# Kernel tuning notes

Hardware: AMD Instinct MI355X
Metric: run time of the kernel (lower is better)

The kernel has to match this reference:

```python
import jax, jax.numpy as jnp
import numpy as np

B, N, D, H, R, K = 64, 197, 768, 3072, 16, 1


def setup_inputs() -> dict:
    key = jax.random.key(0)
    ks = jax.random.split(key, 9)
    s1 = 1.0 / np.sqrt(D)
    s2 = 1.0 / np.sqrt(H)
    return {
        "x": jax.random.normal(ks[0], (B, N, D), dtype=jnp.float32),
        "W1": jax.random.normal(ks[1], (H, D), dtype=jnp.float32) * s1,
        "b1": jax.random.normal(ks[2], (H,), dtype=jnp.float32) * s1,
        "A1": jax.random.normal(ks[3], (K, R, D), dtype=jnp.float32) * s1,
        "B1": jax.random.normal(ks[4], (K, H, R), dtype=jnp.float32) * 0.01,
        "W2": jax.random.normal(ks[5], (D, H), dtype=jnp.float32) * s2,
        "b2": jax.random.normal(ks[6], (D,), dtype=jnp.float32) * s2,
        "A2": jax.random.normal(ks[7], (K, R, H), dtype=jnp.float32) * s2,
        "B2": jax.random.normal(ks[8], (K, D, R), dtype=jnp.float32) * 0.01,
    }


def _lora(x, A, Bm):
    # result of torch: (B @ (A @ x^T.unsqueeze(1))).sum(1).transpose(1,2)
    # A: [K, r, d_in], Bm: [K, d_out, r], x: [b, n, d_in] -> [b, n, d_out]
    t = jnp.einsum('krd,bnd->bknr', A, x)          # low-rank projection
    return jnp.einsum('kor,bknr->bno', Bm, t)      # expand + sum over K


def reference(x, W1, b1, A1, B1, W2, b2, A2, B2):
    # fc1 (Linear + LoRA correction)
    h = jnp.einsum('bnd,hd->bnh', x, W1) + b1 + _lora(x, A1, B1)
    # exact (erf-based) GELU, matching torch nn.GELU default
    h = jax.nn.gelu(h, approximate=False)
    # dropout p=0 and norm=Identity by default -> no-ops
    out = jnp.einsum('bnh,dh->bnd', h, W2) + b2 + _lora(h, A2, B2)
    return out
```

## Files before the change

kernel.cpp:

```cpp
#include <hip/hip_runtime.h>
#include <math.h>

#define M_ROWS 12608
#define D_DIM  768
#define H_DIM  3072

typedef __bf16 bf16_t;
typedef __bf16 bf16x8 __attribute__((ext_vector_type(8)));
typedef float  f32x4  __attribute__((ext_vector_type(4)));

__device__ __forceinline__ float gelu_fast(float v) {
  float v2 = v * v;
  float z = v * fmaf(0.044715f, v2, 1.0f);
  float e = __expf(-1.5957691216057308f * z);
  return v * __builtin_amdgcn_rcpf(1.0f + e);
}

__device__ __forceinline__ void gld16(const bf16_t* g, char* l) {
  __builtin_amdgcn_global_load_lds(
      (const __attribute__((address_space(1))) void*)g,
      (__attribute__((address_space(3))) void*)l, 16, 0, 0);
}

__global__ void cast_f32_bf16_kernel(const float* __restrict__ in,
                                     bf16_t* __restrict__ out, long n) {
  long i = ((long)blockIdx.x * 256 + threadIdx.x) * 4;
  if (i + 3 < n) {
    float4 v = *(const float4*)(in + i);
    out[i + 0] = (bf16_t)v.x; out[i + 1] = (bf16_t)v.y;
    out[i + 2] = (bf16_t)v.z; out[i + 3] = (bf16_t)v.w;
  } else {
    for (; i < n; ++i) out[i] = (bf16_t)in[i];
  }
}

__global__ void fold_lora_kernel(const float* __restrict__ W,
                                 const float* __restrict__ A,
                                 const float* __restrict__ Bm,
                                 bf16_t* __restrict__ Weff,
                                 int OUT, int IN) {
  long idx = (long)blockIdx.x * 256 + threadIdx.x;
  if (idx >= (long)OUT * IN) return;
  int o = (int)(idx / IN);
  int i = (int)(idx - (long)o * IN);
  float s = W[idx];
#pragma unroll
  for (int r = 0; r < 16; ++r)
    s += Bm[o * 16 + r] * A[r * IN + i];
  Weff[idx] = (bf16_t)s;
}

template <bool GELU, typename OutT, int SCHED, int SMEM_BYTES>
__global__ __launch_bounds__(256, 3) void gemm_kernel(
    const bf16_t* __restrict__ Amat, const bf16_t* __restrict__ Bmat,
    const float* __restrict__ bias, OutT* __restrict__ Cmat,
    int Mrows, int Ncols, int Kd) {
  __shared__ char smem[SMEM_BYTES];
  bf16_t* lds = (bf16_t*)smem;
  float* sT = (float*)smem;

  int rowb, colb;
  const int xcd = blockIdx.x & 7, t = blockIdx.x >> 3;
  if (SCHED == 1) {
    colb = t / 13;
    rowb = (t % 13) * 8 + xcd;
    if (rowb >= 99) return;
  } else {
    rowb = (t / 3) * 4 + (xcd & 3);
    if (rowb >= 99) return;
    colb = (xcd >> 2) * 3 + (t % 3);
  }
  const int row0 = rowb * 128, col0 = colb * 128;

  const int tid = threadIdx.x, lane = tid & 63, wave = tid >> 6;
  const int wm = wave & 1, wn = wave >> 1;

  const bf16_t* gA[4]; const bf16_t* gB[4];
  int ldsA[4], ldsB[4];
#pragma unroll
  for (int q = 0; q < 4; ++q) {
    int c = tid + q * 256;
    int r = c >> 3, kkg = (c & 7) ^ (r & 7);
    int ra = row0 + r; if (ra > Mrows - 1) ra = Mrows - 1;
    gA[q] = Amat + (size_t)ra * Kd + kkg * 8;
    gB[q] = Bmat + (size_t)(col0 + r) * Kd + kkg * 8;
    ldsA[q] = c * 16;
    ldsB[q] = 16384 + c * 16;
  }

  const int rl = lane & 15, kc = lane >> 4;
  int aoffs[4], boffs[4];
#pragma unroll
  for (int i = 0; i < 4; ++i) {
    int ra = wm * 64 + i * 16 + rl;
    int rb = wn * 64 + i * 16 + rl;
    aoffs[i] = ra * 64 + ((kc ^ (ra & 7)) * 8);
    boffs[i] = 8192 + rb * 64 + ((kc ^ (rb & 7)) * 8);
  }

  f32x4 acc[4][4] = {};
  const int iters = Kd / 64;

#pragma unroll
  for (int q = 0; q < 4; ++q) {
    gld16(gA[q], smem + ldsA[q]);
    gld16(gB[q], smem + ldsB[q]);
    gA[q] += 64; gB[q] += 64;
  }
  __syncthreads();

  for (int it = 0; it < iters; ++it) {
#pragma unroll
    for (int ks = 0; ks < 2; ++ks) {
      bf16x8 af[4], bfr[4];
#pragma unroll
      for (int i = 0; i < 4; ++i) af[i] = *(const bf16x8*)(lds + (aoffs[i] ^ (ks * 32)));
#pragma unroll
      for (int i = 0; i < 4; ++i) bfr[i] = *(const bf16x8*)(lds + (boffs[i] ^ (ks * 32)));
#pragma unroll
      for (int mi = 0; mi < 4; ++mi)
#pragma unroll
        for (int ni = 0; ni < 4; ++ni)
          acc[mi][ni] = __builtin_amdgcn_mfma_f32_16x16x32_bf16(
              af[mi], bfr[ni], acc[mi][ni], 0, 0, 0);
    }
    if (it + 1 < iters) {
      __syncthreads();
#pragma unroll
      for (int q = 0; q < 4; ++q) {
        gld16(gA[q], smem + ldsA[q]);
        gld16(gB[q], smem + ldsB[q]);
        gA[q] += 64; gB[q] += 64;
      }
      __syncthreads();
    }
  }

  const int crow = (lane >> 4) * 4, ccol = lane & 15;
  if constexpr (GELU) {
    __syncthreads();
#pragma unroll
    for (int p = 0; p < 2; ++p) {
#pragma unroll
      for (int s = 0; s < 2; ++s) {
        int mi = 2 * p + s;
#pragma unroll
        for (int ni = 0; ni < 4; ++ni)
#pragma unroll
          for (int r = 0; r < 4; ++r)
            sT[(wm * 32 + s * 16 + crow + r) * 132 + wn * 64 + ni * 16 + ccol] =
                acc[mi][ni][r];
      }
      __syncthreads();
      const int erow = tid >> 2, eseg = tid & 3;
      const int grow = row0 + (erow >> 5) * 64 + (2 * p + ((erow >> 4) & 1)) * 16 + (erow & 15);
      if (grow < Mrows) {
        const float* src = sT + erow * 132 + eseg * 32;
        const float* bsrc = bias + col0 + eseg * 32;
        bf16_t ov[32];
#pragma unroll
        for (int i = 0; i < 32; ++i)
          ov[i] = (bf16_t)gelu_fast(src[i] + bsrc[i]);
        bf16_t* dst = (bf16_t*)Cmat + (size_t)grow * Ncols + col0 + eseg * 32;
#pragma unroll
        for (int k = 0; k < 4; ++k)
          *(bf16x8*)(dst + k * 8) = *(bf16x8*)(ov + k * 8);
      }
      __syncthreads();
    }
  } else {
#pragma unroll
    for (int ni = 0; ni < 4; ++ni) {
      const int gc = col0 + wn * 64 + ni * 16 + ccol;
      const float bv = bias[gc];
#pragma unroll
      for (int mi = 0; mi < 4; ++mi) {
        const int gr = row0 + wm * 64 + mi * 16 + crow;
#pragma unroll
        for (int r = 0; r < 4; ++r) {
          const int row = gr + r;
          if (row < Mrows)
            Cmat[(size_t)row * Ncols + gc] = acc[mi][ni][r] + bv;
        }
      }
    }
  }
}

extern "C" void kernel_launch(void* const* d_in, const int* in_sizes, int n_in,
                              void* d_out, int out_size, void* d_ws, size_t ws_size,
                              hipStream_t stream) {
  const float* x  = (const float*)d_in[0];
  const float* W1 = (const float*)d_in[1];
  const float* b1 = (const float*)d_in[2];
  const float* A1 = (const float*)d_in[3];
  const float* B1 = (const float*)d_in[4];
  const float* W2 = (const float*)d_in[5];
  const float* b2 = (const float*)d_in[6];
  const float* A2 = (const float*)d_in[7];
  const float* B2 = (const float*)d_in[8];
  float* out = (float*)d_out;

  char* ws = (char*)d_ws;
  bf16_t* xb    = (bf16_t*)ws;
  bf16_t* W1eff = (bf16_t*)(ws + 19366144);
  bf16_t* W2eff = (bf16_t*)(ws + 19366144 + 4718592);
  bf16_t* hbuf  = (bf16_t*)(ws + 19366144 + 2 * 4718592);

  const long nx = (long)M_ROWS * D_DIM;
  cast_f32_bf16_kernel<<<(int)((nx / 4 + 255) / 256), 256, 0, stream>>>(x, xb, nx);

  const int foldBlocks = (H_DIM * D_DIM + 255) / 256;
  fold_lora_kernel<<<foldBlocks, 256, 0, stream>>>(W1, A1, B1, W1eff, H_DIM, D_DIM);
  fold_lora_kernel<<<foldBlocks, 256, 0, stream>>>(W2, A2, B2, W2eff, D_DIM, H_DIM);

  gemm_kernel<true, bf16_t, 1, 33792><<<2496, 256, 0, stream>>>(
      xb, W1eff, b1, hbuf, M_ROWS, H_DIM, D_DIM);
  gemm_kernel<false, float, 2, 32768><<<600, 256, 0, stream>>>(
      hbuf, W2eff, b2, out, M_ROWS, D_DIM, H_DIM);
}
```

Baseline: 286.0 us.

## Add triple-buffered 256x128 GEMM1 kernel with split-phase prefetch and setprio

Replaces the first GEMM (the fc1 projection with fused GELU) with a dedicated kernel. It uses a larger 256x128 tile, 512 threads and a three-stage LDS ring filled by direct global-to-LDS loads. Each K step is split into two halves that interleave prefetch issue, explicit waitcnt and barriers, and MFMA bursts raised with s_setprio, to overlap memory traffic with compute and get more reuse per tile. The 144KB of LDS limits each CU to one block, and the hand-placed waitcnt counts must match the number of loads in flight.

```diff
diff --git a/kernel.cpp b/kernel.cpp
--- a/kernel.cpp
+++ b/kernel.cpp
@@ -48,6 +48,162 @@
   for (int r = 0; r < 16; ++r)
     s += Bm[o * 16 + r] * A[r * IN + i];
   Weff[idx] = (bf16_t)s;
+}
+
+__global__ __launch_bounds__(512, 2) void gemm1_kernel(
+    const bf16_t* __restrict__ Amat, const bf16_t* __restrict__ Bmat,
+    const float* __restrict__ bias, bf16_t* __restrict__ Cmat,
+    int Mrows, int Ncols, int Kd) {
+  __shared__ char smem[147456];
+  bf16_t* lds = (bf16_t*)smem;
+  float* sT = (float*)smem;
+
+  const int xcd = blockIdx.x & 7, t = blockIdx.x >> 3;
+  const int colb = xcd * 3 + (t % 3);
+  const int rowb = t / 3;
+  const int row0 = rowb * 256, col0 = colb * 128;
+
+  const int tid = threadIdx.x, lane = tid & 63, wave = tid >> 6;
+  const int wm = wave & 1, wn = wave >> 1;
+
+  const bf16_t* gA[4]; int ldsA[4];
+  const bf16_t* gB[2]; int ldsB[2];
+#pragma unroll
+  for (int q = 0; q < 4; ++q) {
+    int c = tid + q * 512, r = c >> 3, kkg = (c & 7) ^ (r & 7);
+    int ra = row0 + r; if (ra > Mrows - 1) ra = Mrows - 1;
+    gA[q] = Amat + (size_t)ra * Kd + kkg * 8;
+    ldsA[q] = c * 16;
+  }
+#pragma unroll
+  for (int q = 0; q < 2; ++q) {
+    int c = tid + q * 512, r = c >> 3, kkg = (c & 7) ^ (r & 7);
+    gB[q] = Bmat + (size_t)(col0 + r) * Kd + kkg * 8;
+    ldsB[q] = 32768 + c * 16;
+  }
+
+  const int rl = lane & 15, kc = lane >> 4;
+  int aoffs[8], boffs[2];
+#pragma unroll
+  for (int i = 0; i < 8; ++i) {
+    int ra = wm * 128 + i * 16 + rl;
+    aoffs[i] = ra * 64 + ((kc ^ (ra & 7)) * 8);
+  }
+#pragma unroll
+  for (int i = 0; i < 2; ++i) {
+    int rb = wn * 32 + i * 16 + rl;
+    boffs[i] = 16384 + rb * 64 + ((kc ^ (rb & 7)) * 8);
+  }
+
+  f32x4 acc[8][2] = {};
+  const int NT = Kd / 64;
+
+#pragma unroll
+  for (int j = 0; j < 2; ++j) {
+    const int sb = j * 49152;
+#pragma unroll
+    for (int q = 0; q < 4; ++q) { gld16(gA[q], smem + sb + ldsA[q]); gA[q] += 64; }
+#pragma unroll
+    for (int q = 0; q < 2; ++q) { gld16(gB[q], smem + sb + ldsB[q]); gB[q] += 64; }
+  }
+  asm volatile("s_waitcnt vmcnt(6)" ::: "memory");
+  __builtin_amdgcn_sched_barrier(0);
+  __builtin_amdgcn_s_barrier();
+
+  int cbase = 0;
+  int sbyte = 98304;
+
+  for (int it = 0; it < NT; ++it) {
+    const bool st = (it < NT - 2);
+    bf16x8 af[4][2], bfr[2][2];
+
+#pragma unroll
+    for (int mi = 0; mi < 4; ++mi)
+#pragma unroll
+      for (int ks = 0; ks < 2; ++ks)
+        af[mi][ks] = *(const bf16x8*)(lds + cbase + (aoffs[mi] ^ (ks * 32)));
+#pragma unroll
+    for (int ni = 0; ni < 2; ++ni)
+#pragma unroll
+      for (int ks = 0; ks < 2; ++ks)
+        bfr[ni][ks] = *(const bf16x8*)(lds + cbase + (boffs[ni] ^ (ks * 32)));
+    if (st) {
+      gld16(gA[0], smem + sbyte + ldsA[0]); gA[0] += 64;
+      gld16(gA[1], smem + sbyte + ldsA[1]); gA[1] += 64;
+      gld16(gB[0], smem + sbyte + ldsB[0]); gB[0] += 64;
+    }
+    __builtin_amdgcn_s_barrier();
+    asm volatile("s_waitcnt lgkmcnt(0)" ::: "memory");
+    __builtin_amdgcn_sched_barrier(0);
+    __builtin_amdgcn_s_setprio(1);
+#pragma unroll
+    for (int ks = 0; ks < 2; ++ks)
+#pragma unroll
+      for (int mi = 0; mi < 4; ++mi)
+#pragma unroll
+        for (int ni = 0; ni < 2; ++ni)
+          acc[mi][ni] = __builtin_amdgcn_mfma_f32_16x16x32_bf16(
+              af[mi][ks], bfr[ni][ks], acc[mi][ni], 0, 0, 0);
+    __builtin_amdgcn_s_setprio(0);
+    __builtin_amdgcn_s_barrier();
+
+#pragma unroll
+    for (int mi = 0; mi < 4; ++mi)
+#pragma unroll
+      for (int ks = 0; ks < 2; ++ks)
+        af[mi][ks] = *(const bf16x8*)(lds + cbase + (aoffs[mi + 4] ^ (ks * 32)));
+    if (st) {
+      gld16(gA[2], smem + sbyte + ldsA[2]); gA[2] += 64;
+      gld16(gA[3], smem + sbyte + ldsA[3]); gA[3] += 64;
+      gld16(gB[1], smem + sbyte + ldsB[1]); gB[1] += 64;
+    }
+    __builtin_amdgcn_s_barrier();
+    asm volatile("s_waitcnt lgkmcnt(0)" ::: "memory");
+    __builtin_amdgcn_sched_barrier(0);
+    __builtin_amdgcn_s_setprio(1);
+#pragma unroll
+    for (int ks = 0; ks < 2; ++ks)
+#pragma unroll
+      for (int mi = 0; mi < 4; ++mi)
+#pragma unroll
+        for (int ni = 0; ni < 2; ++ni)
+          acc[mi + 4][ni] = __builtin_amdgcn_mfma_f32_16x16x32_bf16(
+              af[mi][ks], bfr[ni][ks], acc[mi + 4][ni], 0, 0, 0);
+    __builtin_amdgcn_s_setprio(0);
+    if (st) { asm volatile("s_waitcnt vmcnt(6)" ::: "memory"); }
+    else    { asm volatile("s_waitcnt vmcnt(0)" ::: "memory"); }
+    __builtin_amdgcn_sched_barrier(0);
+    __builtin_amdgcn_s_barrier();
+
+    cbase += 24576; if (cbase == 73728) cbase = 0;
+    sbyte += 49152; if (sbyte == 147456) sbyte = 0;
+  }
+
+  const int crow = (lane >> 4) * 4, ccol = lane & 15;
+#pragma unroll
+  for (int mi = 0; mi < 8; ++mi)
+#pragma unroll
+    for (int ni = 0; ni < 2; ++ni)
+#pragma unroll
+      for (int r = 0; r < 4; ++r)
+        sT[(wm * 128 + mi * 16 + crow + r) * 132 + wn * 32 + ni * 16 + ccol] =
+            acc[mi][ni][r];
+  __syncthreads();
+  {
+    const int row = tid >> 1, seg = tid & 1;
+    const int gr = row0 + row;
+    if (gr < Mrows) {
+      const float* src = sT + row * 132 + seg * 64;
+      const float* bs = bias + col0 + seg * 64;
+      bf16_t ov[64];
+#pragma unroll
+      for (int i = 0; i < 64; ++i) ov[i] = (bf16_t)gelu_fast(src[i] + bs[i]);
+      bf16_t* dst = Cmat + (size_t)gr * Ncols + col0 + seg * 64;
+#pragma unroll
+      for (int k = 0; k < 8; ++k)
+        *(bf16x8*)(dst + k * 8) = *(bf16x8*)(ov + k * 8);
+    }
+  }
 }
 
 template <bool GELU, typename OutT, int SCHED, int SMEM_BYTES>
@@ -214,7 +370,7 @@
   fold_lora_kernel<<<foldBlocks, 256, 0, stream>>>(W1, A1, B1, W1eff, H_DIM, D_DIM);
   fold_lora_kernel<<<foldBlocks, 256, 0, stream>>>(W2, A2, B2, W2eff, D_DIM, H_DIM);
 
-  gemm_kernel<true, bf16_t, 1, 33792><<<2496, 256, 0, stream>>>(
+  gemm1_kernel<<<1200, 512, 0, stream>>>(
       xb, W1eff, b1, hbuf, M_ROWS, H_DIM, D_DIM);
   gemm_kernel<false, float, 2, 32768><<<600, 256, 0, stream>>>(
       hbuf, W2eff, b2, out, M_ROWS, D_DIM, H_DIM);
```

After: 312.7 us. +9.3%, slower.

## Add 256x256 double-buffered 8-wave GEMM1 kernel with interleaved load/MFMA schedule

Applied to the files above, without the earlier changes.

Replaces the first GEMM (x·W1eff + bias + GELU) with a dedicated 512-thread kernel that uses 256x256 tiles, 128 KB of double-buffered LDS, and explicit sched barriers, waitcnts and setprio so that global-to-LDS loads for the next K step overlap MFMA work in four sub-phases. Larger tiles raise arithmetic intensity and reduce redundant global reads of A and B. The GELU epilogue is restaged through LDS in four passes. The generic gemm kernel is simplified to the non-GELU path used by GEMM2. Risks include lower occupancy, register pressure from 32 accumulators, and tail inefficiency from 50 row blocks against 12608 rows.

```diff
diff --git a/kernel.cpp b/kernel.cpp
--- a/kernel.cpp
+++ b/kernel.cpp
@@ -50,14 +50,180 @@
   Weff[idx] = (bf16_t)s;
 }
 
-template <bool GELU, typename OutT, int SCHED, int SMEM_BYTES>
+__global__ __launch_bounds__(512, 2) void gemm1_256(
+    const bf16_t* __restrict__ Amat, const bf16_t* __restrict__ Bmat,
+    const float* __restrict__ bias, bf16_t* __restrict__ Cmat,
+    int Mrows, int Ncols, int Kd) {
+  __shared__ char smem[131072];
+  bf16_t* lds = (bf16_t*)smem;
+  float* sT = (float*)smem;
+
+  const int xcd = blockIdx.x & 7, t6 = blockIdx.x >> 3;
+  const int wg = xcd * 75 + t6;
+  const int rowb = wg % 50, colb = wg / 50;
+  const int row0 = rowb * 256, col0 = colb * 256;
+
+  const int tid = threadIdx.x, lane = tid & 63, wave = tid >> 6;
+  const int wm = wave & 1, wn = wave >> 1;
+
+  const bf16_t* gA[2]; const bf16_t* gB[2]; int ldsc[2];
+#pragma unroll
+  for (int q = 0; q < 2; ++q) {
+    int c = tid + q * 512;
+    int r = c >> 2, kk = (c & 3) ^ ((r >> 1) & 3);
+    int ra = row0 + r; if (ra > Mrows - 1) ra = Mrows - 1;
+    gA[q] = Amat + (size_t)ra * Kd + kk * 8;
+    gB[q] = Bmat + (size_t)(col0 + r) * Kd + kk * 8;
+    ldsc[q] = c * 16;
+  }
+
+  const int rl = lane & 15, kc = lane >> 4;
+  int aoffs[8], boffs[4];
+#pragma unroll
+  for (int i = 0; i < 8; ++i) {
+    int ra = wm * 128 + i * 16 + rl;
+    aoffs[i] = ra * 32 + ((kc ^ ((ra >> 1) & 3)) * 8);
+  }
+#pragma unroll
+  for (int i = 0; i < 4; ++i) {
+    int rb = wn * 64 + i * 16 + rl;
+    boffs[i] = rb * 32 + ((kc ^ ((rb >> 1) & 3)) * 8);
+  }
+
+  f32x4 acc[8][4] = {};
+  const int NT = Kd / 64;
+  int knext = 0;
+
+#define STAGE_A(kh, sb)  do {                                               \
+    gld16(gA[0] + knext + (kh) * 32, smem + (sb) + (kh) * 16384 + ldsc[0]); \
+    gld16(gA[1] + knext + (kh) * 32, smem + (sb) + (kh) * 16384 + ldsc[1]); \
+  } while (0)
+#define STAGE_B(kh, sb)  do {                                               \
+    gld16(gB[0] + knext + (kh) * 32, smem + (sb) + 32768 + (kh) * 16384 + ldsc[0]); \
+    gld16(gB[1] + knext + (kh) * 32, smem + (sb) + 32768 + (kh) * 16384 + ldsc[1]); \
+  } while (0)
+#define SB __builtin_amdgcn_sched_barrier(0)
+
+  STAGE_B(0, 0); STAGE_A(0, 0); STAGE_B(1, 0); STAGE_A(1, 0);
+  knext = 64;
+  asm volatile("s_waitcnt vmcnt(4)" ::: "memory"); SB;
+  __builtin_amdgcn_s_barrier();
+
+  for (int it = 0; it < NT; ++it) {
+    const bool st = (it + 1 < NT);
+    const int cbe = (it & 1) * 32768;
+    const int sb = ((it + 1) & 1) * 65536;
+    bf16x8 af[8], bfr[2];
+
+#pragma unroll
+    for (int i = 0; i < 8; ++i) af[i] = *(const bf16x8*)(lds + cbe + aoffs[i]);
+#pragma unroll
+    for (int i = 0; i < 2; ++i) bfr[i] = *(const bf16x8*)(lds + cbe + 16384 + boffs[i]);
+    if (st) STAGE_B(0, sb);
+    __builtin_amdgcn_s_barrier();
+    asm volatile("s_waitcnt lgkmcnt(0)" ::: "memory"); SB;
+    __builtin_amdgcn_s_setprio(1);
+#pragma unroll
+    for (int mi = 0; mi < 8; ++mi)
+#pragma unroll
+      for (int ni = 0; ni < 2; ++ni)
+        acc[mi][ni] = __builtin_amdgcn_mfma_f32_16x16x32_bf16(af[mi], bfr[ni], acc[mi][ni], 0, 0, 0);
+    __builtin_amdgcn_s_setprio(0);
+    __builtin_amdgcn_s_barrier();
+
+#pragma unroll
+    for (int i = 0; i < 2; ++i) bfr[i] = *(const bf16x8*)(lds + cbe + 16384 + boffs[i + 2]);
+    if (st) STAGE_A(0, sb);
+    __builtin_amdgcn_s_barrier();
+    asm volatile("s_waitcnt lgkmcnt(0)" ::: "memory"); SB;
+    __builtin_amdgcn_s_setprio(1);
+#pragma unroll
+    for (int mi = 0; mi < 8; ++mi)
+#pragma unroll
+      for (int ni = 0; ni < 2; ++ni)
+        acc[mi][ni + 2] = __builtin_amdgcn_mfma_f32_16x16x32_bf16(af[mi], bfr[ni], acc[mi][ni + 2], 0, 0, 0);
+    __builtin_amdgcn_s_setprio(0);
+    if (st) { asm volatile("s_waitcnt vmcnt(4)" ::: "memory"); }
+    else    { asm volatile("s_waitcnt vmcnt(0)" ::: "memory"); }
+    SB;
+    __builtin_amdgcn_s_barrier();
+
+#pragma unroll
+    for (int i = 0; i < 8; ++i) af[i] = *(const bf16x8*)(lds + cbe + 8192 + aoffs[i]);
+#pragma unroll
+    for (int i = 0; i < 2; ++i) bfr[i] = *(const bf16x8*)(lds + cbe + 16384 + 8192 + boffs[i]);
+    if (st) STAGE_B(1, sb);
+    __builtin_amdgcn_s_barrier();
+    asm volatile("s_waitcnt lgkmcnt(0)" ::: "memory"); SB;
+    __builtin_amdgcn_s_setprio(1);
+#pragma unroll
+    for (int mi = 0; mi < 8; ++mi)
+#pragma unroll
+      for (int ni = 0; ni < 2; ++ni)
+        acc[mi][ni] = __builtin_amdgcn_mfma_f32_16x16x32_bf16(af[mi], bfr[ni], acc[mi][ni], 0, 0, 0);
+    __builtin_amdgcn_s_setprio(0);
+    __builtin_amdgcn_s_barrier();
+
+#pragma unroll
+    for (int i = 0; i < 2; ++i) bfr[i] = *(const bf16x8*)(lds + cbe + 16384 + 8192 + boffs[i + 2]);
+    if (st) STAGE_A(1, sb);
+    __builtin_amdgcn_s_barrier();
+    asm volatile("s_waitcnt lgkmcnt(0)" ::: "memory"); SB;
+    __builtin_amdgcn_s_setprio(1);
+#pragma unroll
+    for (int mi = 0; mi < 8; ++mi)
+#pragma unroll
+      for (int ni = 0; ni < 2; ++ni)
+        acc[mi][ni + 2] = __builtin_amdgcn_mfma_f32_16x16x32_bf16(af[mi], bfr[ni], acc[mi][ni + 2], 0, 0, 0);
+    __builtin_amdgcn_s_setprio(0);
+    if (st) { asm volatile("s_waitcnt vmcnt(4)" ::: "memory"); SB; }
+    __builtin_amdgcn_s_barrier();
+
+    knext += 64;
+  }
+#undef STAGE_A
+#undef STAGE_B
+
+  const int crow = (lane >> 4) * 4, ccol = lane & 15;
+  __syncthreads();
+#pragma unroll
+  for (int p = 0; p < 4; ++p) {
+    if (wm == (p >> 1)) {
+#pragma unroll
+      for (int s = 0; s < 4; ++s) {
+        int mi = (p & 1) * 4 + s;
+#pragma unroll
+        for (int ni = 0; ni < 4; ++ni)
+#pragma unroll
+          for (int r = 0; r < 4; ++r)
+            sT[(s * 16 + crow + r) * 257 + wn * 64 + ni * 16 + ccol] = acc[mi][ni][r];
+      }
+    }
+    __syncthreads();
+    const int lr = tid >> 3, seg = tid & 7;
+    const int grow = row0 + p * 64 + lr;
+    if (grow < Mrows) {
+      const float* src = sT + lr * 257 + seg * 32;
+      const float* bs = bias + col0 + seg * 32;
+      bf16_t ov[32];
+#pragma unroll
+      for (int i = 0; i < 32; ++i) ov[i] = (bf16_t)gelu_fast(src[i] + bs[i]);
+      bf16_t* dst = Cmat + (size_t)grow * Ncols + col0 + seg * 32;
+#pragma unroll
+      for (int k = 0; k < 4; ++k)
+        *(bf16x8*)(dst + k * 8) = *(bf16x8*)(ov + k * 8);
+    }
+    __syncthreads();
+  }
+}
+
+template <int SCHED, int SMEM_BYTES>
 __global__ __launch_bounds__(256, 3) void gemm_kernel(
     const bf16_t* __restrict__ Amat, const bf16_t* __restrict__ Bmat,
-    const float* __restrict__ bias, OutT* __restrict__ Cmat,
+    const float* __restrict__ bias, float* __restrict__ Cmat,
     int Mrows, int Ncols, int Kd) {
   __shared__ char smem[SMEM_BYTES];
   bf16_t* lds = (bf16_t*)smem;
-  float* sT = (float*)smem;
 
   int rowb, colb;
   const int xcd = blockIdx.x & 7, t = blockIdx.x >> 3;
@@ -137,51 +303,18 @@
   }
 
   const int crow = (lane >> 4) * 4, ccol = lane & 15;
-  if constexpr (GELU) {
-    __syncthreads();
-#pragma unroll
-    for (int p = 0; p < 2; ++p) {
-#pragma unroll
-      for (int s = 0; s < 2; ++s) {
-        int mi = 2 * p + s;
-#pragma unroll
-        for (int ni = 0; ni < 4; ++ni)
-#pragma unroll
-          for (int r = 0; r < 4; ++r)
-            sT[(wm * 32 + s * 16 + crow + r) * 132 + wn * 64 + ni * 16 + ccol] =
-                acc[mi][ni][r];
-      }
-      __syncthreads();
-      const int erow = tid >> 2, eseg = tid & 3;
-      const int grow = row0 + (erow >> 5) * 64 + (2 * p + ((erow >> 4) & 1)) * 16 + (erow & 15);
-      if (grow < Mrows) {
-        const float* src = sT + erow * 132 + eseg * 32;
-        const float* bsrc = bias + col0 + eseg * 32;
-        bf16_t ov[32];
-#pragma unroll
-        for (int i = 0; i < 32; ++i)
-          ov[i] = (bf16_t)gelu_fast(src[i] + bsrc[i]);
-        bf16_t* dst = (bf16_t*)Cmat + (size_t)grow * Ncols + col0 + eseg * 32;
-#pragma unroll
-        for (int k = 0; k < 4; ++k)
-          *(bf16x8*)(dst + k * 8) = *(bf16x8*)(ov + k * 8);
-      }
-      __syncthreads();
-    }
-  } else {
-#pragma unroll
-    for (int ni = 0; ni < 4; ++ni) {
-      const int gc = col0 + wn * 64 + ni * 16 + ccol;
-      const float bv = bias[gc];
-#pragma unroll
-      for (int mi = 0; mi < 4; ++mi) {
-        const int gr = row0 + wm * 64 + mi * 16 + crow;
-#pragma unroll
-        for (int r = 0; r < 4; ++r) {
-          const int row = gr + r;
-          if (row < Mrows)
-            Cmat[(size_t)row * Ncols + gc] = acc[mi][ni][r] + bv;
-        }
+#pragma unroll
+  for (int ni = 0; ni < 4; ++ni) {
+    const int gc = col0 + wn * 64 + ni * 16 + ccol;
+    const float bv = bias[gc];
+#pragma unroll
+    for (int mi = 0; mi < 4; ++mi) {
+      const int gr = row0 + wm * 64 + mi * 16 + crow;
+#pragma unroll
+      for (int r = 0; r < 4; ++r) {
+        const int row = gr + r;
+        if (row < Mrows)
+          Cmat[(size_t)row * Ncols + gc] = acc[mi][ni][r] + bv;
       }
     }
   }
@@ -214,8 +347,8 @@
   fold_lora_kernel<<<foldBlocks, 256, 0, stream>>>(W1, A1, B1, W1eff, H_DIM, D_DIM);
   fold_lora_kernel<<<foldBlocks, 256, 0, stream>>>(W2, A2, B2, W2eff, D_DIM, H_DIM);
 
-  gemm_kernel<true, bf16_t, 1, 33792><<<2496, 256, 0, stream>>>(
+  gemm1_256<<<600, 512, 0, stream>>>(
       xb, W1eff, b1, hbuf, M_ROWS, H_DIM, D_DIM);
-  gemm_kernel<false, float, 2, 32768><<<600, 256, 0, stream>>>(
+  gemm_kernel<2, 32768><<<600, 256, 0, stream>>>(
       hbuf, W2eff, b2, out, M_ROWS, D_DIM, H_DIM);
 }
```

New measurement: 317.9 us. 1.11x slower.

## Merge prep kernels into one launch and retile second GEMM to 64-row blocks

Applied to the files above, without the earlier changes.

Combines the x cast and both LoRA weight folds into a single prep kernel, removing two kernel launches. The second GEMM becomes its own kernel with 64x128 tiles, 1200 blocks, a smaller LDS footprint and a launch bound of 4 blocks per CU. This targets poor wave balance and occupancy in the K=3072 GEMM, which had only 600 blocks. The trade-off is less reuse per tile, since each weight tile is loaded twice as often, and the bounds checks on rows are dropped because 12608 divides evenly by 64.

```diff
diff --git a/kernel.cpp b/kernel.cpp
--- a/kernel.cpp
+++ b/kernel.cpp
@@ -22,25 +22,14 @@
       (__attribute__((address_space(3))) void*)l, 16, 0, 0);
 }
 
-__global__ void cast_f32_bf16_kernel(const float* __restrict__ in,
-                                     bf16_t* __restrict__ out, long n) {
-  long i = ((long)blockIdx.x * 256 + threadIdx.x) * 4;
-  if (i + 3 < n) {
-    float4 v = *(const float4*)(in + i);
-    out[i + 0] = (bf16_t)v.x; out[i + 1] = (bf16_t)v.y;
-    out[i + 2] = (bf16_t)v.z; out[i + 3] = (bf16_t)v.w;
-  } else {
-    for (; i < n; ++i) out[i] = (bf16_t)in[i];
-  }
-}
-
-__global__ void fold_lora_kernel(const float* __restrict__ W,
-                                 const float* __restrict__ A,
-                                 const float* __restrict__ Bm,
-                                 bf16_t* __restrict__ Weff,
-                                 int OUT, int IN) {
-  long idx = (long)blockIdx.x * 256 + threadIdx.x;
-  if (idx >= (long)OUT * IN) return;
+#define CAST_BLOCKS 9456
+#define FOLD_BLOCKS 9216
+
+__device__ __forceinline__ void fold_body(const float* __restrict__ W,
+                                          const float* __restrict__ A,
+                                          const float* __restrict__ Bm,
+                                          bf16_t* __restrict__ Weff,
+                                          int IN, long idx) {
   int o = (int)(idx / IN);
   int i = (int)(idx - (long)o * IN);
   float s = W[idx];
@@ -50,26 +39,39 @@
   Weff[idx] = (bf16_t)s;
 }
 
-template <bool GELU, typename OutT, int SCHED, int SMEM_BYTES>
-__global__ __launch_bounds__(256, 3) void gemm_kernel(
+__global__ __launch_bounds__(256) void prep_kernel(
+    const float* __restrict__ x, bf16_t* __restrict__ xb,
+    const float* __restrict__ W1, const float* __restrict__ A1,
+    const float* __restrict__ B1, bf16_t* __restrict__ W1eff,
+    const float* __restrict__ W2, const float* __restrict__ A2,
+    const float* __restrict__ B2, bf16_t* __restrict__ W2eff) {
+  const int b = blockIdx.x;
+  if (b < CAST_BLOCKS) {
+    long i = ((long)b * 256 + threadIdx.x) * 4;
+    float4 v = *(const float4*)(x + i);
+    xb[i + 0] = (bf16_t)v.x; xb[i + 1] = (bf16_t)v.y;
+    xb[i + 2] = (bf16_t)v.z; xb[i + 3] = (bf16_t)v.w;
+  } else if (b < CAST_BLOCKS + FOLD_BLOCKS) {
+    long idx = (long)(b - CAST_BLOCKS) * 256 + threadIdx.x;
+    fold_body(W1, A1, B1, W1eff, D_DIM, idx);
+  } else {
+    long idx = (long)(b - CAST_BLOCKS - FOLD_BLOCKS) * 256 + threadIdx.x;
+    fold_body(W2, A2, B2, W2eff, H_DIM, idx);
+  }
+}
+
+__global__ __launch_bounds__(256, 3) void gemm1_kernel(
     const bf16_t* __restrict__ Amat, const bf16_t* __restrict__ Bmat,
-    const float* __restrict__ bias, OutT* __restrict__ Cmat,
+    const float* __restrict__ bias, bf16_t* __restrict__ Cmat,
     int Mrows, int Ncols, int Kd) {
-  __shared__ char smem[SMEM_BYTES];
+  __shared__ char smem[33792];
   bf16_t* lds = (bf16_t*)smem;
   float* sT = (float*)smem;
 
-  int rowb, colb;
   const int xcd = blockIdx.x & 7, t = blockIdx.x >> 3;
-  if (SCHED == 1) {
-    colb = t / 13;
-    rowb = (t % 13) * 8 + xcd;
-    if (rowb >= 99) return;
-  } else {
-    rowb = (t / 3) * 4 + (xcd & 3);
-    if (rowb >= 99) return;
-    colb = (xcd >> 2) * 3 + (t % 3);
-  }
+  const int colb = t / 13;
+  const int rowb = (t % 13) * 8 + xcd;
+  if (rowb >= 99) return;
   const int row0 = rowb * 128, col0 = colb * 128;
 
   const int tid = threadIdx.x, lane = tid & 63, wave = tid >> 6;
@@ -137,52 +139,129 @@
   }
 
   const int crow = (lane >> 4) * 4, ccol = lane & 15;
-  if constexpr (GELU) {
+  __syncthreads();
+#pragma unroll
+  for (int p = 0; p < 2; ++p) {
+#pragma unroll
+    for (int s = 0; s < 2; ++s) {
+      int mi = 2 * p + s;
+#pragma unroll
+      for (int ni = 0; ni < 4; ++ni)
+#pragma unroll
+        for (int r = 0; r < 4; ++r)
+          sT[(wm * 32 + s * 16 + crow + r) * 132 + wn * 64 + ni * 16 + ccol] =
+              acc[mi][ni][r];
+    }
     __syncthreads();
-#pragma unroll
-    for (int p = 0; p < 2; ++p) {
-#pragma unroll
-      for (int s = 0; s < 2; ++s) {
-        int mi = 2 * p + s;
+    const int erow = tid >> 2, eseg = tid & 3;
+    const int grow = row0 + (erow >> 5) * 64 + (2 * p + ((erow >> 4) & 1)) * 16 + (erow & 15);
+    if (grow < Mrows) {
+      const float* src = sT + erow * 132 + eseg * 32;
+      const float* bsrc = bias + col0 + eseg * 32;
+      bf16_t ov[32];
+#pragma unroll
+      for (int i = 0; i < 32; ++i)
+        ov[i] = (bf16_t)gelu_fast(src[i] + bsrc[i]);
+      bf16_t* dst = Cmat + (size_t)grow * Ncols + col0 + eseg * 32;
+#pragma unroll
+      for (int k = 0; k < 4; ++k)
+        *(bf16x8*)(dst + k * 8) = *(bf16x8*)(ov + k * 8);
+    }
+    __syncthreads();
+  }
+}
+
+__global__ __launch_bounds__(256, 4) void gemm2_kernel(
+    const bf16_t* __restrict__ Amat, const bf16_t* __restrict__ Bmat,
+    const float* __restrict__ bias, float* __restrict__ Cmat,
+    int Mrows, int Ncols, int Kd) {
+  __shared__ char smem[24576];
+  bf16_t* lds = (bf16_t*)smem;
+
+  const int xcd = blockIdx.x & 7, t = blockIdx.x >> 3;
+  const int rowb = (t / 3) * 4 + (xcd & 3);
+  if (rowb >= 197) return;
+  const int colb = (xcd >> 2) * 3 + (t % 3);
+  const int row0 = rowb * 64, col0 = colb * 128;
+
+  const int tid = threadIdx.x, lane = tid & 63, wave = tid >> 6;
+  const int wm = wave & 1, wn = wave >> 1;
+
+  const bf16_t* gA[2]; int ldsA[2];
+  const bf16_t* gB[4]; int ldsB[4];
+#pragma unroll
+  for (int q = 0; q < 2; ++q) {
+    int c = tid + q * 256;
+    int r = c >> 3, kkg = (c & 7) ^ (r & 7);
+    gA[q] = Amat + (size_t)(row0 + r) * Kd + kkg * 8;
+    ldsA[q] = c * 16;
+  }
+#pragma unroll
+  for (int q = 0; q < 4; ++q) {
+    int c = tid + q * 256;
+    int r = c >> 3, kkg = (c & 7) ^ (r & 7);
+    gB[q] = Bmat + (size_t)(col0 + r) * Kd + kkg * 8;
+    ldsB[q] = 8192 + c * 16;
+  }
+
+  const int rl = lane & 15, kc = lane >> 4;
+  int aoffs[2], boffs[4];
+#pragma unroll
+  for (int i = 0; i < 2; ++i) {
+    int ra = wm * 32 + i * 16 + rl;
+    aoffs[i] = ra * 64 + ((kc ^ (ra & 7)) * 8);
+  }
+#pragma unroll
+  for (int i = 0; i < 4; ++i) {
+    int rb = wn * 64 + i * 16 + rl;
+    boffs[i] = 4096 + rb * 64 + ((kc ^ (rb & 7)) * 8);
+  }
+
+  f32x4 acc[2][4] = {};
+  const int iters = Kd / 64;
+
+#pragma unroll
+  for (int q = 0; q < 2; ++q) { gld16(gA[q], smem + ldsA[q]); gA[q] += 64; }
+#pragma unroll
+  for (int q = 0; q < 4; ++q) { gld16(gB[q], smem + ldsB[q]); gB[q] += 64; }
+  __syncthreads();
+
+  for (int it = 0; it < iters; ++it) {
+#pragma unroll
+    for (int ks = 0; ks < 2; ++ks) {
+      bf16x8 af[2], bfr[4];
+#pragma unroll
+      for (int i = 0; i < 2; ++i) af[i] = *(const bf16x8*)(lds + (aoffs[i] ^ (ks * 32)));
+#pragma unroll
+      for (int i = 0; i < 4; ++i) bfr[i] = *(const bf16x8*)(lds + (boffs[i] ^ (ks * 32)));
+#pragma unroll
+      for (int mi = 0; mi < 2; ++mi)
 #pragma unroll
         for (int ni = 0; ni < 4; ++ni)
-#pragma unroll
-          for (int r = 0; r < 4; ++r)
-            sT[(wm * 32 + s * 16 + crow + r) * 132 + wn * 64 + ni * 16 + ccol] =
-                acc[mi][ni][r];
-      }
-      __syncthreads();
-      const int erow = tid >> 2, eseg = tid & 3;
-      const int grow = row0 + (erow >> 5) * 64 + (2 * p + ((erow >> 4) & 1)) * 16 + (erow & 15);
-      if (grow < Mrows) {
-        const float* src = sT + erow * 132 + eseg * 32;
-        const float* bsrc = bias + col0 + eseg * 32;
-        bf16_t ov[32];
-#pragma unroll
-        for (int i = 0; i < 32; ++i)
-          ov[i] = (bf16_t)gelu_fast(src[i] + bsrc[i]);
-        bf16_t* dst = (bf16_t*)Cmat + (size_t)grow * Ncols + col0 + eseg * 32;
-#pragma unroll
-        for (int k = 0; k < 4; ++k)
-          *(bf16x8*)(dst + k * 8) = *(bf16x8*)(ov + k * 8);
-      }
-      __syncthreads();
-    }
-  } else {
-#pragma unroll
-    for (int ni = 0; ni < 4; ++ni) {
-      const int gc = col0 + wn * 64 + ni * 16 + ccol;
-      const float bv = bias[gc];
-#pragma unroll
-      for (int mi = 0; mi < 4; ++mi) {
-        const int gr = row0 + wm * 64 + mi * 16 + crow;
-#pragma unroll
-        for (int r = 0; r < 4; ++r) {
-          const int row = gr + r;
-          if (row < Mrows)
-            Cmat[(size_t)row * Ncols + gc] = acc[mi][ni][r] + bv;
-        }
-      }
+          acc[mi][ni] = __builtin_amdgcn_mfma_f32_16x16x32_bf16(
+              af[mi], bfr[ni], acc[mi][ni], 0, 0, 0);
+    }
+    if (it + 1 < iters) {
+      __syncthreads();
+#pragma unroll
+      for (int q = 0; q < 2; ++q) { gld16(gA[q], smem + ldsA[q]); gA[q] += 64; }
+#pragma unroll
+      for (int q = 0; q < 4; ++q) { gld16(gB[q], smem + ldsB[q]); gB[q] += 64; }
+      __syncthreads();
+    }
+  }
+
+  const int crow = (lane >> 4) * 4, ccol = lane & 15;
+#pragma unroll
+  for (int ni = 0; ni < 4; ++ni) {
+    const int gc = col0 + wn * 64 + ni * 16 + ccol;
+    const float bv = bias[gc];
+#pragma unroll
+    for (int mi = 0; mi < 2; ++mi) {
+      const int gr = row0 + wm * 32 + mi * 16 + crow;
+#pragma unroll
+      for (int r = 0; r < 4; ++r)
+        Cmat[(size_t)(gr + r) * Ncols + gc] = acc[mi][ni][r] + bv;
     }
   }
 }
@@ -207,15 +286,11 @@
   bf16_t* W2eff = (bf16_t*)(ws + 19366144 + 4718592);
   bf16_t* hbuf  = (bf16_t*)(ws + 19366144 + 2 * 4718592);
 
-  const long nx = (long)M_ROWS * D_DIM;
-  cast_f32_bf16_kernel<<<(int)((nx / 4 + 255) / 256), 256, 0, stream>>>(x, xb, nx);
-
-  const int foldBlocks = (H_DIM * D_DIM + 255) / 256;
-  fold_lora_kernel<<<foldBlocks, 256, 0, stream>>>(W1, A1, B1, W1eff, H_DIM, D_DIM);
-  fold_lora_kernel<<<foldBlocks, 256, 0, stream>>>(W2, A2, B2, W2eff, D_DIM, H_DIM);
-
-  gemm_kernel<true, bf16_t, 1, 33792><<<2496, 256, 0, stream>>>(
+  prep_kernel<<<CAST_BLOCKS + 2 * FOLD_BLOCKS, 256, 0, stream>>>(
+      x, xb, W1, A1, B1, W1eff, W2, A2, B2, W2eff);
+
+  gemm1_kernel<<<2496, 256, 0, stream>>>(
       xb, W1eff, b1, hbuf, M_ROWS, H_DIM, D_DIM);
-  gemm_kernel<false, float, 2, 32768><<<600, 256, 0, stream>>>(
+  gemm2_kernel<<<1200, 256, 0, stream>>>(
       hbuf, W2eff, b2, out, M_ROWS, D_DIM, H_DIM);
 }
```

Measured after the change: 286.2 us. No clear change (+0.1%).
